# Kernel optimization log

Hardware: AMD Instinct MI355X
Metric: run time of the kernel (lower is better)

Reference implementation:

```python
import jax, jax.numpy as jnp
import numpy as np

D = 16       # data dimension
M = 64       # hidden width
ALPHA0 = 1.0 # alpha[0]
H_RES = 1.0  # ResNet step h = 1/(n_layers-1), n_layers=2


def _antideriv_tanh(x):
    # log(exp(x)+exp(-x)), numerically stable
    return jnp.abs(x) + jnp.log1p(jnp.exp(-2.0 * jnp.abs(x)))


def _dtanh(x):
    t = jnp.tanh(x)
    return 1.0 - t * t


def grad_and_hessian_trace(s, w, A, b, K0, b0, K1, b1):
    """OT-Flow analytic grad of Phi and trace of Hessian (w.r.t. first d coords).
    s: (n, d+1) = [x; t]. n_layers=2 -> one residual layer, h=1."""
    d = s.shape[1] - 1
    opening = s @ K0.T + b0                         # (n, m)
    u0 = _antideriv_tanh(opening)                   # (n, m)
    feat1 = u0 @ K1.T + b1                          # (n, m)
    tanhopen = jnp.tanh(opening)                    # (n, m)
    # backward pass for gradient: z1 = w + h K1^T (tanh(feat1) * w)
    z1 = w + H_RES * (jnp.tanh(feat1) * w) @ K1     # (n, m)
    z0 = (tanhopen * z1) @ K0                       # (n, d+1)
    symA = A.T @ A                                  # (d+1, d+1)
    grad = z0 + s @ symA + b                        # (n, d+1)
    # Hessian trace: opening-layer term
    Kopen = K0[:, :d]                               # (m, d)
    trH = (_dtanh(opening) * z1) @ jnp.sum(Kopen**2, axis=1)   # (n,)
    # forward-propagated Jacobian of u0 w.r.t. x: (n, m, d)
    Jac = tanhopen[:, :, None] * Kopen[None, :, :]
    KJ = jnp.einsum('ij,njd->nid', K1, Jac)         # (n, m, d)
    t1 = jnp.einsum('nm,nmd->n', _dtanh(feat1) * w, KJ**2)
    trH = trH + H_RES * t1 + jnp.sum(A[:, :d] ** 2)  # + trace(symA[:d,:d])
    return grad, trH


def odefun(z, t, w, A, b, K0, b0, K1, b1):
    n = z.shape[0]
    x = z[:, :D]
    s = jnp.concatenate([x, jnp.full((n, 1), t, dtype=z.dtype)], axis=1)
    gradPhi, trH = grad_and_hessian_trace(s, w, A, b, K0, b0, K1, b1)
    dx = -(1.0 / ALPHA0) * gradPhi[:, :D]
    dl = -(1.0 / ALPHA0) * trH[:, None]
    dv = 0.5 * jnp.sum(dx * dx, axis=1, keepdims=True)
    dr = jnp.abs(-gradPhi[:, -1:] + ALPHA0 * dv)
    return jnp.concatenate([dx, dl, dv, dr], axis=1)


def step_rk4(f, z, t0, t1):
    h = t1 - t0
    z0 = z
    K = h * f(z0, t0)
    z = z0 + K / 6.0
    K = h * f(z0 + 0.5 * K, t0 + 0.5 * h)
    z = z + K / 3.0
    K = h * f(z0 + 0.5 * K, t0 + 0.5 * h)
    z = z + K / 3.0
    K = h * f(z0 + K, t0 + h)
    z = z + K / 6.0
    return z


def setup_inputs() -> dict:
    key = jax.random.key(0)
    ks = jax.random.split(key, 8)
    n = 32768
    dp1 = D + 1
    x = jax.random.normal(ks[0], (n, D), dtype=jnp.float32)
    w = jax.random.normal(ks[1], (M,), dtype=jnp.float32) / np.sqrt(M)
    A = 0.1 * jax.random.normal(ks[2], (10, dp1), dtype=jnp.float32)
    b = 0.1 * jax.random.normal(ks[3], (dp1,), dtype=jnp.float32)
    K0 = jax.random.normal(ks[4], (M, dp1), dtype=jnp.float32) / np.sqrt(dp1)
    b0 = 0.1 * jax.random.normal(ks[5], (M,), dtype=jnp.float32)
    K1 = jax.random.normal(ks[6], (M, M), dtype=jnp.float32) / np.sqrt(M)
    b1 = 0.1 * jax.random.normal(ks[7], (M,), dtype=jnp.float32)
    return {"x": x, "w": w, "A": A, "b": b, "K0": K0, "b0": b0,
            "K1": K1, "b1": b1, "nt": 8}


def reference(x, w, A, b, K0, b0, K1, b1, nt):
    f = lambda z, t: odefun(z, t, w, A, b, K0, b0, K1, b1)
    h = 1.0 / nt
    z = jnp.concatenate([x, jnp.zeros((x.shape[0], 3), x.dtype)], axis=1)
    for k in range(nt):  # nt is a static python int
        z = step_rk4(f, z, k * h, (k + 1) * h)
    # unpack: (x_latent, log_det, transport_cost, hjb_violation)
    return z[:, :D], z[:, D], z[:, D + 1], z[:, D + 2]
```

## Files before the change

### kernel.cpp

```cpp
#include <hip/hip_runtime.h>
#include <math.h>

typedef __attribute__((ext_vector_type(8))) short bf16x8;
typedef __attribute__((ext_vector_type(4))) float f32x4;

union B8 { bf16x8 v; unsigned u[4]; };

__device__ __forceinline__ unsigned pk2(float lo, float hi) {
  unsigned r;
  asm("v_cvt_pk_bf16_f32 %0, %1, %2" : "=v"(r) : "v"(lo), "v"(hi));
  return r;
}
__device__ __forceinline__ float rcpf(float x) { return __builtin_amdgcn_rcpf(x); }
__device__ __forceinline__ void ldsfence() { asm volatile("s_waitcnt lgkmcnt(0)" ::: "memory"); }

#define MFMA __builtin_amdgcn_mfma_f32_16x16x32_bf16

__global__ void otflow_prep(const float* __restrict__ K0g,
                            const float* __restrict__ Ag,
                            float* __restrict__ ws) {
  __shared__ float Als[170];
  int tid = threadIdx.x;
  for (int idx = tid; idx < 1024; idx += 256) {
    int m = idx >> 4, d = idx & 15;
    ws[idx] = K0g[m * 17 + d];
  }
  if (tid < 170) Als[tid] = Ag[tid];
  if (tid < 64) {
    float s = 0.f;
    for (int d = 0; d < 16; ++d) { float v = K0g[tid * 17 + d]; s += v * v; }
    ws[1320 + tid] = s;
  }
  __syncthreads();
  for (int idx = tid; idx < 289; idx += 256) {
    int j = idx / 17, k2 = idx % 17;
    float s = 0.f;
#pragma unroll
    for (int r = 0; r < 10; ++r) s += Als[r * 17 + j] * Als[r * 17 + k2];
    ws[1024 + idx] = s;
  }
  __syncthreads();
  if (tid == 0) {
    float s = 0.f;
    for (int r = 0; r < 10; ++r)
      for (int j = 0; j < 16; ++j) { float v = Als[r * 17 + j]; s += v * v; }
    ws[1313] = s;
  }
}

__global__ __launch_bounds__(64, 2) void otflow_main(
    const float* __restrict__ xg, const float* __restrict__ wg,
    const float* __restrict__ bg, const float* __restrict__ K0g,
    const float* __restrict__ b0g, const float* __restrict__ K1g,
    const float* __restrict__ b1g, const int* __restrict__ ntg,
    const float* __restrict__ ws, float* __restrict__ out, int n) {
  __shared__ float buf[16 * 68];
  __shared__ float csh[16 * 68];
  __shared__ float qsh[16 * 68];
  __shared__ float tsh[16 * 20];
  __shared__ float b1s[64], wss[64], k0qs[64], b0s[64], tcs[64];

  const int lane = threadIdx.x;
  const int lr = lane & 15;
  const int lg = lane >> 4;

  b1s[lane] = b1g[lane];
  wss[lane] = wg[lane];
  k0qs[lane] = ws[1320 + lane];
  b0s[lane] = b0g[lane];
  tcs[lane] = K0g[lane * 17 + 16];

  const float sumA2 = ws[1313];

  B8 aK0[4], aK0L[4], aK1[8], aK1T[8], aG[6];
  float kop[16];
#pragma unroll
  for (int mi = 0; mi < 4; ++mi) {
    B8 th, tl;
#pragma unroll
    for (int jj = 0; jj < 4; ++jj) {
      float e0 = K0g[(mi * 16 + lr) * 17 + (lg & 1) * 8 + jj * 2];
      float e1 = K0g[(mi * 16 + lr) * 17 + (lg & 1) * 8 + jj * 2 + 1];
      unsigned hh = pk2(e0, e1);
      th.u[jj] = hh;
      float l0 = e0 - __uint_as_float(hh << 16);
      float l1 = e1 - __uint_as_float(hh & 0xffff0000u);
      tl.u[jj] = pk2(l0, l1);
    }
    aK0[mi] = th; aK0L[mi] = tl;
  }
#pragma unroll
  for (int mi = 0; mi < 4; ++mi)
#pragma unroll
    for (int kb = 0; kb < 2; ++kb) {
      const float* pp = K1g + (mi * 16 + lr) * 64 + kb * 32 + lg * 8;
      float4 q0 = *(const float4*)pp;
      float4 q1 = *(const float4*)(pp + 4);
      B8 t;
      t.u[0] = pk2(q0.x, q0.y); t.u[1] = pk2(q0.z, q0.w);
      t.u[2] = pk2(q1.x, q1.y); t.u[3] = pk2(q1.z, q1.w);
      aK1[mi * 2 + kb] = t;
    }
#pragma unroll
  for (int mi = 0; mi < 4; ++mi)
#pragma unroll
    for (int kb = 0; kb < 2; ++kb) {
      int ib = kb * 32 + lg * 8;
      int m = mi * 16 + lr;
      B8 t;
#pragma unroll
      for (int jj = 0; jj < 4; ++jj)
        t.u[jj] = pk2(K1g[(ib + jj * 2) * 64 + m], K1g[(ib + jj * 2 + 1) * 64 + m]);
      aK1T[mi * 2 + kb] = t;
    }
#pragma unroll
  for (int nb = 0; nb < 2; ++nb)
#pragma unroll
    for (int kb = 0; kb < 3; ++kb) {
      int j = nb * 16 + lr; if (j > 16) j = 16;
      float e[8];
#pragma unroll
      for (int jj = 0; jj < 8; ++jj) {
        float v;
        if (kb < 2) v = K0g[(kb * 32 + lg * 8 + jj) * 17 + j];
        else {
          int kr = lg * 8 + jj;
          v = (kr < 17) ? ws[1024 + kr * 17 + j] : (kr == 17) ? bg[j] : 0.f;
        }
        e[jj] = v;
      }
      B8 t;
      t.u[0] = pk2(e[0], e[1]); t.u[1] = pk2(e[2], e[3]);
      t.u[2] = pk2(e[4], e[5]); t.u[3] = pk2(e[6], e[7]);
      aG[nb * 3 + kb] = t;
    }
#pragma unroll
  for (int kb = 0; kb < 2; ++kb)
#pragma unroll
    for (int j = 0; j < 8; ++j)
      kop[kb * 8 + j] = ws[(kb * 32 + lg * 8 + j) * 16 + lr];

  ldsfence();

  const int nt = *ntg;
  const float h = 1.0f / (float)nt;
  const int p0 = blockIdx.x * 16;
  int pidx = p0 + lr; if (pidx >= n) pidx = n - 1;

  float xin[4], x0s[4], xac[4];
  {
    float4 xi = *(const float4*)(xg + (size_t)pidx * 16 + lg * 4);
    xin[0] = xi.x; xin[1] = xi.y; xin[2] = xi.z; xin[3] = xi.w;
#pragma unroll
    for (int r = 0; r < 4; ++r) { x0s[r] = xin[r]; xac[r] = xin[r]; }
  }
  float lacc = 0.f, vacc = 0.f, racc = 0.f;
  const f32x4 zz = {0.f, 0.f, 0.f, 0.f};

  for (int kstep = 0; kstep < nt; ++kstep) {
    float t0 = (float)kstep * h;
#pragma unroll 1
    for (int st = 0; st < 4; ++st) {
      float tin = t0 + ((st == 0) ? 0.f : (st == 3) ? h : 0.5f * h);

      { float4 xv = {xin[0], xin[1], xin[2], xin[3]};
        *(float4*)(buf + lr * 68 + lg * 4) = xv; }
      ldsfence();
      float4 s0 = *(const float4*)(buf + lr * 68 + (lg & 1) * 8);
      float4 s1 = *(const float4*)(buf + lr * 68 + (lg & 1) * 8 + 4);
      unsigned h0 = pk2(s0.x, s0.y), h1 = pk2(s0.z, s0.w);
      unsigned h2 = pk2(s1.x, s1.y), h3 = pk2(s1.z, s1.w);
      B8 sfO, sfG;
      if (lg < 2) {
        sfO.u[0] = h0; sfO.u[1] = h1; sfO.u[2] = h2; sfO.u[3] = h3;
        sfG.u[0] = h0; sfG.u[1] = h1; sfG.u[2] = h2; sfG.u[3] = h3;
      } else {
        float l0 = s0.x - __uint_as_float(h0 << 16);
        float l1 = s0.y - __uint_as_float(h0 & 0xffff0000u);
        float l2 = s0.z - __uint_as_float(h1 << 16);
        float l3 = s0.w - __uint_as_float(h1 & 0xffff0000u);
        float l4 = s1.x - __uint_as_float(h2 << 16);
        float l5 = s1.y - __uint_as_float(h2 & 0xffff0000u);
        float l6 = s1.z - __uint_as_float(h3 << 16);
        float l7 = s1.w - __uint_as_float(h3 & 0xffff0000u);
        sfO.u[0] = pk2(l0, l1); sfO.u[1] = pk2(l2, l3);
        sfO.u[2] = pk2(l4, l5); sfO.u[3] = pk2(l6, l7);
        if (lg == 2) { sfG.u[0] = pk2(tin, 1.f); sfG.u[1] = 0; sfG.u[2] = 0; sfG.u[3] = 0; }
        else { sfG.u[0] = 0; sfG.u[1] = 0; sfG.u[2] = 0; sfG.u[3] = 0; }
      }

      f32x4 o0 = MFMA(aK0[0].v, sfO.v, zz, 0, 0, 0);
      f32x4 o1 = MFMA(aK0[1].v, sfO.v, zz, 0, 0, 0);
      f32x4 o2 = MFMA(aK0[2].v, sfO.v, zz, 0, 0, 0);
      f32x4 o3 = MFMA(aK0[3].v, sfO.v, zz, 0, 0, 0);
      o0 = MFMA(aK0L[0].v, sfO.v, o0, 0, 0, 0);
      o1 = MFMA(aK0L[1].v, sfO.v, o1, 0, 0, 0);
      o2 = MFMA(aK0L[2].v, sfO.v, o2, 0, 0, 0);
      o3 = MFMA(aK0L[3].v, sfO.v, o3, 0, 0, 0);

      float cva[16];
#pragma unroll
      for (int mi = 0; mi < 4; ++mi) {
        f32x4 oa = (mi == 0) ? o0 : (mi == 1) ? o1 : (mi == 2) ? o2 : o3;
        float4 b0v = *(const float4*)(b0s + mi * 16 + lg * 4);
        float4 tcv = *(const float4*)(tcs + mi * 16 + lg * 4);
        float4 u0v;
#pragma unroll
        for (int r = 0; r < 4; ++r) {
          float ov = oa[r] + fmaf(tin, ((const float*)&tcv)[r], ((const float*)&b0v)[r]);
          float e = __expf(-2.f * fabsf(ov));
          float rp = rcpf(1.f + e);
          float cm = (1.f - e) * rp;
          cva[mi * 4 + r] = __builtin_copysignf(cm, ov);
          ((float*)&u0v)[r] = fabsf(ov) + __logf(1.f + e);
        }
        *(float4*)(buf + lr * 68 + mi * 16 + lg * 4) = u0v;
      }
      ldsfence();

      B8 uf0, uf1;
      {
        const float* bp = buf + lr * 68;
        float4 a0 = *(const float4*)(bp + lg * 8);
        float4 a1 = *(const float4*)(bp + lg * 8 + 4);
        float4 a2 = *(const float4*)(bp + 32 + lg * 8);
        float4 a3 = *(const float4*)(bp + 32 + lg * 8 + 4);
        uf0.u[0] = pk2(a0.x, a0.y); uf0.u[1] = pk2(a0.z, a0.w);
        uf0.u[2] = pk2(a1.x, a1.y); uf0.u[3] = pk2(a1.z, a1.w);
        uf1.u[0] = pk2(a2.x, a2.y); uf1.u[1] = pk2(a2.z, a2.w);
        uf1.u[2] = pk2(a3.x, a3.y); uf1.u[3] = pk2(a3.z, a3.w);
      }
      f32x4 f0 = MFMA(aK1[0].v, uf0.v, zz, 0, 0, 0); f0 = MFMA(aK1[1].v, uf1.v, f0, 0, 0, 0);
      f32x4 f1 = MFMA(aK1[2].v, uf0.v, zz, 0, 0, 0); f1 = MFMA(aK1[3].v, uf1.v, f1, 0, 0, 0);
      f32x4 f2 = MFMA(aK1[4].v, uf0.v, zz, 0, 0, 0); f2 = MFMA(aK1[5].v, uf1.v, f2, 0, 0, 0);
      f32x4 f3 = MFMA(aK1[6].v, uf0.v, zz, 0, 0, 0); f3 = MFMA(aK1[7].v, uf1.v, f3, 0, 0, 0);

#pragma unroll
      for (int mi = 0; mi < 4; ++mi) {
        f32x4 fa = (mi == 0) ? f0 : (mi == 1) ? f1 : (mi == 2) ? f2 : f3;
        float4 b1v = *(const float4*)(b1s + mi * 16 + lg * 4);
        float4 wv = *(const float4*)(wss + mi * 16 + lg * 4);
        float4 av4, qv4;
#pragma unroll
        for (int r = 0; r < 4; ++r) {
          float fv = fa[r] + ((const float*)&b1v)[r];
          float e = __expf(-2.f * fabsf(fv));
          float rp = rcpf(1.f + e);
          float tf = __builtin_copysignf((1.f - e) * rp, fv);
          float wr = ((const float*)&wv)[r];
          ((float*)&av4)[r] = tf * wr;
          ((float*)&qv4)[r] = (1.f - tf * tf) * wr;
        }
        *(float4*)(buf + lr * 68 + mi * 16 + lg * 4) = av4;
        *(float4*)(qsh + lr * 68 + mi * 16 + lg * 4) = qv4;
      }
      ldsfence();

      B8 af0, af1;
      {
        const float* bp = buf + lr * 68;
        float4 a0 = *(const float4*)(bp + lg * 8);
        float4 a1 = *(const float4*)(bp + lg * 8 + 4);
        float4 a2 = *(const float4*)(bp + 32 + lg * 8);
        float4 a3 = *(const float4*)(bp + 32 + lg * 8 + 4);
        af0.u[0] = pk2(a0.x, a0.y); af0.u[1] = pk2(a0.z, a0.w);
        af0.u[2] = pk2(a1.x, a1.y); af0.u[3] = pk2(a1.z, a1.w);
        af1.u[0] = pk2(a2.x, a2.y); af1.u[1] = pk2(a2.z, a2.w);
        af1.u[2] = pk2(a3.x, a3.y); af1.u[3] = pk2(a3.z, a3.w);
      }
      f32x4 z0 = MFMA(aK1T[0].v, af0.v, zz, 0, 0, 0); z0 = MFMA(aK1T[1].v, af1.v, z0, 0, 0, 0);
      f32x4 z1 = MFMA(aK1T[2].v, af0.v, zz, 0, 0, 0); z1 = MFMA(aK1T[3].v, af1.v, z1, 0, 0, 0);
      f32x4 z2 = MFMA(aK1T[4].v, af0.v, zz, 0, 0, 0); z2 = MFMA(aK1T[5].v, af1.v, z2, 0, 0, 0);
      f32x4 z3 = MFMA(aK1T[6].v, af0.v, zz, 0, 0, 0); z3 = MFMA(aK1T[7].v, af1.v, z3, 0, 0, 0);

      float trh_l = 0.f;
#pragma unroll
      for (int mi = 0; mi < 4; ++mi) {
        f32x4 za = (mi == 0) ? z0 : (mi == 1) ? z1 : (mi == 2) ? z2 : z3;
        float4 wv = *(const float4*)(wss + mi * 16 + lg * 4);
        float4 kq = *(const float4*)(k0qs + mi * 16 + lg * 4);
        float4 rv4, cv4;
#pragma unroll
        for (int r = 0; r < 4; ++r) {
          float c = cva[mi * 4 + r];
          float z1v = za[r] + ((const float*)&wv)[r];
          ((float*)&rv4)[r] = c * z1v;
          float dt0 = 1.f - c * c;
          trh_l = fmaf(dt0 * z1v, ((const float*)&kq)[r], trh_l);
          ((float*)&cv4)[r] = c;
        }
        *(float4*)(buf + lr * 68 + mi * 16 + lg * 4) = rv4;
        *(float4*)(csh + lr * 68 + mi * 16 + lg * 4) = cv4;
      }
      trh_l += __shfl_xor(trh_l, 16, 64);
      trh_l += __shfl_xor(trh_l, 32, 64);
      ldsfence();

#pragma unroll 2
      for (int p = 0; p < 16; ++p) {
        const float* cp = csh + p * 68;
        float4 ca = *(const float4*)(cp + lg * 8);
        float4 cb = *(const float4*)(cp + lg * 8 + 4);
        float4 cc = *(const float4*)(cp + 32 + lg * 8);
        float4 cd = *(const float4*)(cp + 32 + lg * 8 + 4);
        B8 y0, y1;
        y0.u[0] = pk2(ca.x * kop[0], ca.y * kop[1]);
        y0.u[1] = pk2(ca.z * kop[2], ca.w * kop[3]);
        y0.u[2] = pk2(cb.x * kop[4], cb.y * kop[5]);
        y0.u[3] = pk2(cb.z * kop[6], cb.w * kop[7]);
        y1.u[0] = pk2(cc.x * kop[8], cc.y * kop[9]);
        y1.u[1] = pk2(cc.z * kop[10], cc.w * kop[11]);
        y1.u[2] = pk2(cd.x * kop[12], cd.y * kop[13]);
        y1.u[3] = pk2(cd.z * kop[14], cd.w * kop[15]);
        f32x4 kc0 = MFMA(y0.v, aK1[0].v, zz, 0, 0, 0); kc0 = MFMA(y1.v, aK1[1].v, kc0, 0, 0, 0);
        f32x4 kc1 = MFMA(y0.v, aK1[2].v, zz, 0, 0, 0); kc1 = MFMA(y1.v, aK1[3].v, kc1, 0, 0, 0);
        f32x4 kc2 = MFMA(y0.v, aK1[4].v, zz, 0, 0, 0); kc2 = MFMA(y1.v, aK1[5].v, kc2, 0, 0, 0);
        f32x4 kc3 = MFMA(y0.v, aK1[6].v, zz, 0, 0, 0); kc3 = MFMA(y1.v, aK1[7].v, kc3, 0, 0, 0);
        float q0 = qsh[p * 68 + lr];
        float q1 = qsh[p * 68 + 16 + lr];
        float q2 = qsh[p * 68 + 32 + lr];
        float q3 = qsh[p * 68 + 48 + lr];
        float d0 = kc0[0] * kc0[0] + kc0[1] * kc0[1] + kc0[2] * kc0[2] + kc0[3] * kc0[3];
        float d1 = kc1[0] * kc1[0] + kc1[1] * kc1[1] + kc1[2] * kc1[2] + kc1[3] * kc1[3];
        float d2 = kc2[0] * kc2[0] + kc2[1] * kc2[1] + kc2[2] * kc2[2] + kc2[3] * kc2[3];
        float d3 = kc3[0] * kc3[0] + kc3[1] * kc3[1] + kc3[2] * kc3[2] + kc3[3] * kc3[3];
        float tp = q0 * d0 + q1 * d1 + q2 * d2 + q3 * d3;
        tp += __shfl_xor(tp, 16, 64);
        tp += __shfl_xor(tp, 32, 64);
        if (lg == 0) tsh[p * 20 + lr] = tp;
      }
      ldsfence();
      float4 tv = *(const float4*)(tsh + lr * 20 + lg * 4);
      float tsum = tv.x + tv.y + tv.z + tv.w;
      tsum += __shfl_xor(tsum, 16, 64);
      tsum += __shfl_xor(tsum, 32, 64);

      B8 rf0, rf1;
      {
        const float* bp = buf + lr * 68;
        float4 a0 = *(const float4*)(bp + lg * 8);
        float4 a1 = *(const float4*)(bp + lg * 8 + 4);
        float4 a2 = *(const float4*)(bp + 32 + lg * 8);
        float4 a3 = *(const float4*)(bp + 32 + lg * 8 + 4);
        rf0.u[0] = pk2(a0.x, a0.y); rf0.u[1] = pk2(a0.z, a0.w);
        rf0.u[2] = pk2(a1.x, a1.y); rf0.u[3] = pk2(a1.z, a1.w);
        rf1.u[0] = pk2(a2.x, a2.y); rf1.u[1] = pk2(a2.z, a2.w);
        rf1.u[2] = pk2(a3.x, a3.y); rf1.u[3] = pk2(a3.z, a3.w);
      }
      f32x4 g0 = MFMA(aG[0].v, rf0.v, zz, 0, 0, 0);
      g0 = MFMA(aG[1].v, rf1.v, g0, 0, 0, 0);
      g0 = MFMA(aG[2].v, sfG.v, g0, 0, 0, 0);
      f32x4 g1 = MFMA(aG[3].v, rf0.v, zz, 0, 0, 0);
      g1 = MFMA(aG[4].v, rf1.v, g1, 0, 0, 0);
      g1 = MFMA(aG[5].v, sfG.v, g1, 0, 0, 0);

      float kx[4];
      float dvp = 0.f;
#pragma unroll
      for (int r = 0; r < 4; ++r) { float d = -g0[r]; kx[r] = d; dvp = fmaf(d, d, dvp); }
      dvp += __shfl_xor(dvp, 16, 64);
      dvp += __shfl_xor(dvp, 32, 64);
      dvp *= 0.5f;
      float g16 = g1[0];
      float trH = trh_l + tsum + sumA2;
      float dl = -trH;
      float dr = fabsf(dvp - g16);
      float wch = ((st == 0 || st == 3) ? (1.f / 6.f) : (1.f / 3.f)) * h;
#pragma unroll
      for (int r = 0; r < 4; ++r) xac[r] = fmaf(wch, kx[r], xac[r]);
      lacc = fmaf(wch, dl, lacc);
      vacc = fmaf(wch, dvp, vacc);
      racc = fmaf(wch, dr, racc);
      if (st < 3) {
        float anh = ((st == 2) ? 1.f : 0.5f) * h;
#pragma unroll
        for (int r = 0; r < 4; ++r) xin[r] = fmaf(anh, kx[r], x0s[r]);
      } else {
#pragma unroll
        for (int r = 0; r < 4; ++r) { x0s[r] = xac[r]; xin[r] = xac[r]; }
      }
    }
  }

  if (p0 + lr < n) {
    float4 xa = {xac[0], xac[1], xac[2], xac[3]};
    *(float4*)(out + (size_t)(p0 + lr) * 16 + lg * 4) = xa;
    if (lg == 0) {
      out[(size_t)n * 16 + p0 + lr] = lacc;
      out[(size_t)n * 17 + p0 + lr] = vacc;
      out[(size_t)n * 18 + p0 + lr] = racc;
    }
  }
}

extern "C" void kernel_launch(void* const* d_in, const int* in_sizes, int n_in,
                              void* d_out, int out_size, void* d_ws, size_t ws_size,
                              hipStream_t stream) {
  const float* xg = (const float*)d_in[0];
  const float* wg = (const float*)d_in[1];
  const float* Ag = (const float*)d_in[2];
  const float* bg = (const float*)d_in[3];
  const float* K0g = (const float*)d_in[4];
  const float* b0g = (const float*)d_in[5];
  const float* K1g = (const float*)d_in[6];
  const float* b1g = (const float*)d_in[7];
  const int* ntg = (const int*)d_in[8];
  float* out = (float*)d_out;
  float* ws = (float*)d_ws;
  int n = in_sizes[0] / 16;

  hipLaunchKernelGGL(otflow_prep, dim3(1), dim3(256), 0, stream, K0g, Ag, ws);
  int nblk = (n + 15) / 16;
  hipLaunchKernelGGL(otflow_main, dim3(nblk), dim3(64), 0, stream,
                     xg, wg, bg, K0g, b0g, K1g, b1g, ntg, ws, out, n);
}
```

Measured before the change: 358.3 us.

## Split each block into two waves of eight samples with shared K0 fragments in LDS

Result: slower. 689.7 us (+92.5%).

```diff
diff --git a/kernel.cpp b/kernel.cpp
--- a/kernel.cpp
+++ b/kernel.cpp
@@ -3,12 +3,19 @@
 
 typedef __attribute__((ext_vector_type(8))) short bf16x8;
 typedef __attribute__((ext_vector_type(4))) float f32x4;
-
-union B8 { bf16x8 v; unsigned u[4]; };
+typedef __attribute__((ext_vector_type(2))) float f32x2;
+typedef __attribute__((ext_vector_type(4))) unsigned u32x4;
+
+union B8 { bf16x8 v; unsigned u[4]; u32x4 q; };
 
 __device__ __forceinline__ unsigned pk2(float lo, float hi) {
   unsigned r;
   asm("v_cvt_pk_bf16_f32 %0, %1, %2" : "=v"(r) : "v"(lo), "v"(hi));
+  return r;
+}
+__device__ __forceinline__ f32x2 pkmul(f32x2 a, f32x2 b) {
+  f32x2 r;
+  asm("v_pk_mul_f32 %0, %1, %2" : "=v"(r) : "v"(a), "v"(b));
   return r;
 }
 __device__ __forceinline__ float rcpf(float x) { return __builtin_amdgcn_rcpf(x); }
@@ -48,47 +55,57 @@
   }
 }
 
-__global__ __launch_bounds__(64, 2) void otflow_main(
+__global__ __launch_bounds__(128, 3) void otflow_main(
     const float* __restrict__ xg, const float* __restrict__ wg,
     const float* __restrict__ bg, const float* __restrict__ K0g,
     const float* __restrict__ b0g, const float* __restrict__ K1g,
     const float* __restrict__ b1g, const int* __restrict__ ntg,
     const float* __restrict__ ws, float* __restrict__ out, int n) {
-  __shared__ float buf[16 * 68];
-  __shared__ float csh[16 * 68];
-  __shared__ float qsh[16 * 68];
-  __shared__ float tsh[16 * 20];
-  __shared__ float b1s[64], wss[64], k0qs[64], b0s[64], tcs[64];
-
-  const int lane = threadIdx.x;
+  __shared__ unsigned aK0lds[8 * 64 * 4];
+  __shared__ unsigned Xu[2][8 * 36];
+  __shared__ float csh[2][8 * 68];
+  __shared__ float qsh[2][8 * 68];
+  __shared__ float gsh[2][8 * 20];
+  __shared__ float tshv[2][8];
+  __shared__ float b0s[64], tcs[64], b1s[64], wss[64], k0qs[64], scol[18];
+
+  const int tid = threadIdx.x;
+  const int wid = tid >> 6;
+  const int lane = tid & 63;
   const int lr = lane & 15;
   const int lg = lane >> 4;
-
-  b1s[lane] = b1g[lane];
-  wss[lane] = wg[lane];
-  k0qs[lane] = ws[1320 + lane];
-  b0s[lane] = b0g[lane];
-  tcs[lane] = K0g[lane * 17 + 16];
+  const int p8 = lr & 7;
+  const bool own = (lr < 8);
+
+  if (wid == 0) {
+    b0s[lane] = b0g[lane];
+    tcs[lane] = K0g[lane * 17 + 16];
+    b1s[lane] = b1g[lane];
+    wss[lane] = wg[lane];
+    k0qs[lane] = ws[1320 + lane];
+    if (lane < 17) scol[lane] = ws[1024 + lane * 17 + 16];
+    if (lane == 17) scol[17] = bg[16];
+#pragma unroll
+    for (int mi = 0; mi < 4; ++mi) {
+      unsigned th[4], tl[4];
+#pragma unroll
+      for (int jj = 0; jj < 4; ++jj) {
+        float e0 = K0g[(mi * 16 + lr) * 17 + (lg & 1) * 8 + jj * 2];
+        float e1 = K0g[(mi * 16 + lr) * 17 + (lg & 1) * 8 + jj * 2 + 1];
+        unsigned hh = pk2(e0, e1);
+        th[jj] = hh;
+        float l0 = e0 - __uint_as_float(hh << 16);
+        float l1 = e1 - __uint_as_float(hh & 0xffff0000u);
+        tl[jj] = pk2(l0, l1);
+      }
+      *(u32x4*)(aK0lds + (mi * 64 + lane) * 4) = (u32x4){th[0], th[1], th[2], th[3]};
+      *(u32x4*)(aK0lds + ((4 + mi) * 64 + lane) * 4) = (u32x4){tl[0], tl[1], tl[2], tl[3]};
+    }
+  }
 
   const float sumA2 = ws[1313];
 
-  B8 aK0[4], aK0L[4], aK1[8], aK1T[8], aG[6];
-  float kop[16];
-#pragma unroll
-  for (int mi = 0; mi < 4; ++mi) {
-    B8 th, tl;
-#pragma unroll
-    for (int jj = 0; jj < 4; ++jj) {
-      float e0 = K0g[(mi * 16 + lr) * 17 + (lg & 1) * 8 + jj * 2];
-      float e1 = K0g[(mi * 16 + lr) * 17 + (lg & 1) * 8 + jj * 2 + 1];
-      unsigned hh = pk2(e0, e1);
-      th.u[jj] = hh;
-      float l0 = e0 - __uint_as_float(hh << 16);
-      float l1 = e1 - __uint_as_float(hh & 0xffff0000u);
-      tl.u[jj] = pk2(l0, l1);
-    }
-    aK0[mi] = th; aK0L[mi] = tl;
-  }
+  B8 aK1[8];
 #pragma unroll
   for (int mi = 0; mi < 4; ++mi)
 #pragma unroll
@@ -101,23 +118,24 @@
       t.u[2] = pk2(q1.x, q1.y); t.u[3] = pk2(q1.z, q1.w);
       aK1[mi * 2 + kb] = t;
     }
+  B8 aK1T[8];
 #pragma unroll
   for (int mi = 0; mi < 4; ++mi)
 #pragma unroll
     for (int kb = 0; kb < 2; ++kb) {
       int ib = kb * 32 + lg * 8;
       int m = mi * 16 + lr;
-      B8 t;
+      B8 tt;
 #pragma unroll
       for (int jj = 0; jj < 4; ++jj)
-        t.u[jj] = pk2(K1g[(ib + jj * 2) * 64 + m], K1g[(ib + jj * 2 + 1) * 64 + m]);
-      aK1T[mi * 2 + kb] = t;
-    }
-#pragma unroll
-  for (int nb = 0; nb < 2; ++nb)
+        tt.u[jj] = pk2(K1g[(ib + jj * 2) * 64 + m], K1g[(ib + jj * 2 + 1) * 64 + m]);
+      aK1T[mi * 2 + kb] = tt;
+    }
+  B8 aG0[3];
+  {
+    int j = lr;
 #pragma unroll
     for (int kb = 0; kb < 3; ++kb) {
-      int j = nb * 16 + lr; if (j > 16) j = 16;
       float e[8];
 #pragma unroll
       for (int jj = 0; jj < 8; ++jj) {
@@ -132,20 +150,29 @@
       B8 t;
       t.u[0] = pk2(e[0], e[1]); t.u[1] = pk2(e[2], e[3]);
       t.u[2] = pk2(e[4], e[5]); t.u[3] = pk2(e[6], e[7]);
-      aG[nb * 3 + kb] = t;
-    }
+      aG0[kb] = t;
+    }
+  }
+  f32x2 kop2[8];
 #pragma unroll
   for (int kb = 0; kb < 2; ++kb)
 #pragma unroll
-    for (int j = 0; j < 8; ++j)
-      kop[kb * 8 + j] = ws[(kb * 32 + lg * 8 + j) * 16 + lr];
-
-  ldsfence();
+    for (int j = 0; j < 4; ++j) {
+      f32x2 t;
+      t.x = ws[(kb * 32 + lg * 8 + 2 * j) * 16 + lr];
+      t.y = ws[(kb * 32 + lg * 8 + 2 * j + 1) * 16 + lr];
+      kop2[kb * 4 + j] = t;
+    }
+
+  __syncthreads();
+
+  float4 sc4 = *(const float4*)(scol + lg * 4);
+  const float sc16 = scol[16], sc17 = scol[17];
 
   const int nt = *ntg;
   const float h = 1.0f / (float)nt;
-  const int p0 = blockIdx.x * 16;
-  int pidx = p0 + lr; if (pidx >= n) pidx = n - 1;
+  const int pbase = blockIdx.x * 16 + wid * 8;
+  int pidx = pbase + p8; if (pidx >= n) pidx = n - 1;
 
   float xin[4], x0s[4], xac[4];
   {
@@ -156,6 +183,11 @@
   }
   float lacc = 0.f, vacc = 0.f, racc = 0.f;
   const f32x4 zz = {0.f, 0.f, 0.f, 0.f};
+
+  unsigned* Xw = Xu[wid];
+  float* cw = csh[wid];
+  float* qw = qsh[wid];
+  float* gw = gsh[wid];
 
   for (int kstep = 0; kstep < nt; ++kstep) {
     float t0 = (float)kstep * h;
@@ -163,11 +195,14 @@
     for (int st = 0; st < 4; ++st) {
       float tin = t0 + ((st == 0) ? 0.f : (st == 3) ? h : 0.5f * h);
 
-      { float4 xv = {xin[0], xin[1], xin[2], xin[3]};
-        *(float4*)(buf + lr * 68 + lg * 4) = xv; }
+      if (own) {
+        float4 xv = {xin[0], xin[1], xin[2], xin[3]};
+        *(float4*)(cw + p8 * 68 + lg * 4) = xv;
+      }
       ldsfence();
-      float4 s0 = *(const float4*)(buf + lr * 68 + (lg & 1) * 8);
-      float4 s1 = *(const float4*)(buf + lr * 68 + (lg & 1) * 8 + 4);
+      const float* sp = cw + p8 * 68;
+      float4 s0 = *(const float4*)(sp + (lg & 1) * 8);
+      float4 s1 = *(const float4*)(sp + (lg & 1) * 8 + 4);
       unsigned h0 = pk2(s0.x, s0.y), h1 = pk2(s0.z, s0.w);
       unsigned h2 = pk2(s1.x, s1.y), h3 = pk2(s1.z, s1.w);
       B8 sfO, sfG;
@@ -189,179 +224,168 @@
         else { sfG.u[0] = 0; sfG.u[1] = 0; sfG.u[2] = 0; sfG.u[3] = 0; }
       }
 
-      f32x4 o0 = MFMA(aK0[0].v, sfO.v, zz, 0, 0, 0);
-      f32x4 o1 = MFMA(aK0[1].v, sfO.v, zz, 0, 0, 0);
-      f32x4 o2 = MFMA(aK0[2].v, sfO.v, zz, 0, 0, 0);
-      f32x4 o3 = MFMA(aK0[3].v, sfO.v, zz, 0, 0, 0);
-      o0 = MFMA(aK0L[0].v, sfO.v, o0, 0, 0, 0);
-      o1 = MFMA(aK0L[1].v, sfO.v, o1, 0, 0, 0);
-      o2 = MFMA(aK0L[2].v, sfO.v, o2, 0, 0, 0);
-      o3 = MFMA(aK0L[3].v, sfO.v, o3, 0, 0, 0);
-
-      float cva[16];
-#pragma unroll
-      for (int mi = 0; mi < 4; ++mi) {
-        f32x4 oa = (mi == 0) ? o0 : (mi == 1) ? o1 : (mi == 2) ? o2 : o3;
+      B8 k0f[8];
+#pragma unroll
+      for (int f = 0; f < 8; ++f) k0f[f].q = *(const u32x4*)(aK0lds + (f * 64 + lane) * 4);
+      f32x4 oA[4];
+#pragma unroll
+      for (int mi = 0; mi < 4; ++mi) {
+        oA[mi] = MFMA(k0f[mi].v, sfO.v, zz, 0, 0, 0);
+        oA[mi] = MFMA(k0f[4 + mi].v, sfO.v, oA[mi], 0, 0, 0);
+      }
+#pragma unroll
+      for (int mi = 0; mi < 4; ++mi) {
         float4 b0v = *(const float4*)(b0s + mi * 16 + lg * 4);
         float4 tcv = *(const float4*)(tcs + mi * 16 + lg * 4);
-        float4 u0v;
+        float u0v[4], cv[4];
 #pragma unroll
         for (int r = 0; r < 4; ++r) {
-          float ov = oa[r] + fmaf(tin, ((const float*)&tcv)[r], ((const float*)&b0v)[r]);
+          float ov = oA[mi][r] + fmaf(tin, ((const float*)&tcv)[r], ((const float*)&b0v)[r]);
           float e = __expf(-2.f * fabsf(ov));
           float rp = rcpf(1.f + e);
-          float cm = (1.f - e) * rp;
-          cva[mi * 4 + r] = __builtin_copysignf(cm, ov);
-          ((float*)&u0v)[r] = fabsf(ov) + __logf(1.f + e);
-        }
-        *(float4*)(buf + lr * 68 + mi * 16 + lg * 4) = u0v;
+          cv[r] = __builtin_copysignf((1.f - e) * rp, ov);
+          u0v[r] = fabsf(ov) + __logf(1.f + e);
+        }
+        unsigned ua = pk2(u0v[0], u0v[1]), ub = pk2(u0v[2], u0v[3]);
+        if (own) {
+          *(uint2*)(Xw + p8 * 36 + mi * 8 + lg * 2) = make_uint2(ua, ub);
+          float4 cf = {cv[0], cv[1], cv[2], cv[3]};
+          *(float4*)(cw + p8 * 68 + mi * 16 + lg * 4) = cf;
+        }
       }
       ldsfence();
 
       B8 uf0, uf1;
-      {
-        const float* bp = buf + lr * 68;
-        float4 a0 = *(const float4*)(bp + lg * 8);
-        float4 a1 = *(const float4*)(bp + lg * 8 + 4);
-        float4 a2 = *(const float4*)(bp + 32 + lg * 8);
-        float4 a3 = *(const float4*)(bp + 32 + lg * 8 + 4);
-        uf0.u[0] = pk2(a0.x, a0.y); uf0.u[1] = pk2(a0.z, a0.w);
-        uf0.u[2] = pk2(a1.x, a1.y); uf0.u[3] = pk2(a1.z, a1.w);
-        uf1.u[0] = pk2(a2.x, a2.y); uf1.u[1] = pk2(a2.z, a2.w);
-        uf1.u[2] = pk2(a3.x, a3.y); uf1.u[3] = pk2(a3.z, a3.w);
-      }
-      f32x4 f0 = MFMA(aK1[0].v, uf0.v, zz, 0, 0, 0); f0 = MFMA(aK1[1].v, uf1.v, f0, 0, 0, 0);
-      f32x4 f1 = MFMA(aK1[2].v, uf0.v, zz, 0, 0, 0); f1 = MFMA(aK1[3].v, uf1.v, f1, 0, 0, 0);
-      f32x4 f2 = MFMA(aK1[4].v, uf0.v, zz, 0, 0, 0); f2 = MFMA(aK1[5].v, uf1.v, f2, 0, 0, 0);
-      f32x4 f3 = MFMA(aK1[6].v, uf0.v, zz, 0, 0, 0); f3 = MFMA(aK1[7].v, uf1.v, f3, 0, 0, 0);
-
-#pragma unroll
-      for (int mi = 0; mi < 4; ++mi) {
-        f32x4 fa = (mi == 0) ? f0 : (mi == 1) ? f1 : (mi == 2) ? f2 : f3;
+      uf0.q = *(const u32x4*)(Xw + p8 * 36 + lg * 4);
+      uf1.q = *(const u32x4*)(Xw + p8 * 36 + 16 + lg * 4);
+      f32x4 fA[4];
+#pragma unroll
+      for (int mi = 0; mi < 4; ++mi) {
+        fA[mi] = MFMA(aK1[mi * 2].v, uf0.v, zz, 0, 0, 0);
+        fA[mi] = MFMA(aK1[mi * 2 + 1].v, uf1.v, fA[mi], 0, 0, 0);
+      }
+#pragma unroll
+      for (int mi = 0; mi < 4; ++mi) {
         float4 b1v = *(const float4*)(b1s + mi * 16 + lg * 4);
         float4 wv = *(const float4*)(wss + mi * 16 + lg * 4);
-        float4 av4, qv4;
+        float av[4], qv[4];
 #pragma unroll
         for (int r = 0; r < 4; ++r) {
-          float fv = fa[r] + ((const float*)&b1v)[r];
+          float fv = fA[mi][r] + ((const float*)&b1v)[r];
           float e = __expf(-2.f * fabsf(fv));
           float rp = rcpf(1.f + e);
           float tf = __builtin_copysignf((1.f - e) * rp, fv);
           float wr = ((const float*)&wv)[r];
-          ((float*)&av4)[r] = tf * wr;
-          ((float*)&qv4)[r] = (1.f - tf * tf) * wr;
-        }
-        *(float4*)(buf + lr * 68 + mi * 16 + lg * 4) = av4;
-        *(float4*)(qsh + lr * 68 + mi * 16 + lg * 4) = qv4;
+          av[r] = tf * wr;
+          qv[r] = (1.f - tf * tf) * wr;
+        }
+        unsigned pa = pk2(av[0], av[1]), pb = pk2(av[2], av[3]);
+        if (own) {
+          *(uint2*)(Xw + p8 * 36 + mi * 8 + lg * 2) = make_uint2(pa, pb);
+          float4 qf = {qv[0], qv[1], qv[2], qv[3]};
+          *(float4*)(qw + p8 * 68 + mi * 16 + lg * 4) = qf;
+        }
       }
       ldsfence();
 
       B8 af0, af1;
-      {
-        const float* bp = buf + lr * 68;
-        float4 a0 = *(const float4*)(bp + lg * 8);
-        float4 a1 = *(const float4*)(bp + lg * 8 + 4);
-        float4 a2 = *(const float4*)(bp + 32 + lg * 8);
-        float4 a3 = *(const float4*)(bp + 32 + lg * 8 + 4);
-        af0.u[0] = pk2(a0.x, a0.y); af0.u[1] = pk2(a0.z, a0.w);
-        af0.u[2] = pk2(a1.x, a1.y); af0.u[3] = pk2(a1.z, a1.w);
-        af1.u[0] = pk2(a2.x, a2.y); af1.u[1] = pk2(a2.z, a2.w);
-        af1.u[2] = pk2(a3.x, a3.y); af1.u[3] = pk2(a3.z, a3.w);
-      }
-      f32x4 z0 = MFMA(aK1T[0].v, af0.v, zz, 0, 0, 0); z0 = MFMA(aK1T[1].v, af1.v, z0, 0, 0, 0);
-      f32x4 z1 = MFMA(aK1T[2].v, af0.v, zz, 0, 0, 0); z1 = MFMA(aK1T[3].v, af1.v, z1, 0, 0, 0);
-      f32x4 z2 = MFMA(aK1T[4].v, af0.v, zz, 0, 0, 0); z2 = MFMA(aK1T[5].v, af1.v, z2, 0, 0, 0);
-      f32x4 z3 = MFMA(aK1T[6].v, af0.v, zz, 0, 0, 0); z3 = MFMA(aK1T[7].v, af1.v, z3, 0, 0, 0);
-
-      float trh_l = 0.f;
-#pragma unroll
-      for (int mi = 0; mi < 4; ++mi) {
-        f32x4 za = (mi == 0) ? z0 : (mi == 1) ? z1 : (mi == 2) ? z2 : z3;
+      af0.q = *(const u32x4*)(Xw + p8 * 36 + lg * 4);
+      af1.q = *(const u32x4*)(Xw + p8 * 36 + 16 + lg * 4);
+      f32x4 zA[4];
+#pragma unroll
+      for (int mi = 0; mi < 4; ++mi) {
+        zA[mi] = MFMA(aK1T[mi * 2].v, af0.v, zz, 0, 0, 0);
+        zA[mi] = MFMA(aK1T[mi * 2 + 1].v, af1.v, zA[mi], 0, 0, 0);
+      }
+      float trh_l = 0.f, g16p = 0.f;
+#pragma unroll
+      for (int mi = 0; mi < 4; ++mi) {
         float4 wv = *(const float4*)(wss + mi * 16 + lg * 4);
         float4 kq = *(const float4*)(k0qs + mi * 16 + lg * 4);
-        float4 rv4, cv4;
+        float4 tcv = *(const float4*)(tcs + mi * 16 + lg * 4);
+        float4 cv4 = *(const float4*)(cw + p8 * 68 + mi * 16 + lg * 4);
+        float rv[4];
 #pragma unroll
         for (int r = 0; r < 4; ++r) {
-          float c = cva[mi * 4 + r];
-          float z1v = za[r] + ((const float*)&wv)[r];
-          ((float*)&rv4)[r] = c * z1v;
-          float dt0 = 1.f - c * c;
-          trh_l = fmaf(dt0 * z1v, ((const float*)&kq)[r], trh_l);
-          ((float*)&cv4)[r] = c;
-        }
-        *(float4*)(buf + lr * 68 + mi * 16 + lg * 4) = rv4;
-        *(float4*)(csh + lr * 68 + mi * 16 + lg * 4) = cv4;
-      }
+          float c = ((const float*)&cv4)[r];
+          float z1v = zA[mi][r] + ((const float*)&wv)[r];
+          rv[r] = c * z1v;
+          trh_l = fmaf((1.f - c * c) * z1v, ((const float*)&kq)[r], trh_l);
+          g16p = fmaf(rv[r], ((const float*)&tcv)[r], g16p);
+        }
+        unsigned ra = pk2(rv[0], rv[1]), rb = pk2(rv[2], rv[3]);
+        if (own) *(uint2*)(Xw + p8 * 36 + mi * 8 + lg * 2) = make_uint2(ra, rb);
+      }
+#pragma unroll
+      for (int r = 0; r < 4; ++r) g16p = fmaf(xin[r], ((const float*)&sc4)[r], g16p);
       trh_l += __shfl_xor(trh_l, 16, 64);
       trh_l += __shfl_xor(trh_l, 32, 64);
+      g16p += __shfl_xor(g16p, 16, 64);
+      g16p += __shfl_xor(g16p, 32, 64);
+      float g16 = g16p + fmaf(tin, sc16, sc17);
       ldsfence();
 
 #pragma unroll 2
-      for (int p = 0; p < 16; ++p) {
-        const float* cp = csh + p * 68;
+      for (int p = 0; p < 8; ++p) {
+        const float* cp = cw + p * 68;
         float4 ca = *(const float4*)(cp + lg * 8);
         float4 cb = *(const float4*)(cp + lg * 8 + 4);
         float4 cc = *(const float4*)(cp + 32 + lg * 8);
         float4 cd = *(const float4*)(cp + 32 + lg * 8 + 4);
         B8 y0, y1;
-        y0.u[0] = pk2(ca.x * kop[0], ca.y * kop[1]);
-        y0.u[1] = pk2(ca.z * kop[2], ca.w * kop[3]);
-        y0.u[2] = pk2(cb.x * kop[4], cb.y * kop[5]);
-        y0.u[3] = pk2(cb.z * kop[6], cb.w * kop[7]);
-        y1.u[0] = pk2(cc.x * kop[8], cc.y * kop[9]);
-        y1.u[1] = pk2(cc.z * kop[10], cc.w * kop[11]);
-        y1.u[2] = pk2(cd.x * kop[12], cd.y * kop[13]);
-        y1.u[3] = pk2(cd.z * kop[14], cd.w * kop[15]);
+        f32x2 pr;
+        pr = pkmul((f32x2){ca.x, ca.y}, kop2[0]); y0.u[0] = pk2(pr.x, pr.y);
+        pr = pkmul((f32x2){ca.z, ca.w}, kop2[1]); y0.u[1] = pk2(pr.x, pr.y);
+        pr = pkmul((f32x2){cb.x, cb.y}, kop2[2]); y0.u[2] = pk2(pr.x, pr.y);
+        pr = pkmul((f32x2){cb.z, cb.w}, kop2[3]); y0.u[3] = pk2(pr.x, pr.y);
+        pr = pkmul((f32x2){cc.x, cc.y}, kop2[4]); y1.u[0] = pk2(pr.x, pr.y);
+        pr = pkmul((f32x2){cc.z, cc.w}, kop2[5]); y1.u[1] = pk2(pr.x, pr.y);
+        pr = pkmul((f32x2){cd.x, cd.y}, kop2[6]); y1.u[2] = pk2(pr.x, pr.y);
+        pr = pkmul((f32x2){cd.z, cd.w}, kop2[7]); y1.u[3] = pk2(pr.x, pr.y);
         f32x4 kc0 = MFMA(y0.v, aK1[0].v, zz, 0, 0, 0); kc0 = MFMA(y1.v, aK1[1].v, kc0, 0, 0, 0);
         f32x4 kc1 = MFMA(y0.v, aK1[2].v, zz, 0, 0, 0); kc1 = MFMA(y1.v, aK1[3].v, kc1, 0, 0, 0);
         f32x4 kc2 = MFMA(y0.v, aK1[4].v, zz, 0, 0, 0); kc2 = MFMA(y1.v, aK1[5].v, kc2, 0, 0, 0);
         f32x4 kc3 = MFMA(y0.v, aK1[6].v, zz, 0, 0, 0); kc3 = MFMA(y1.v, aK1[7].v, kc3, 0, 0, 0);
-        float q0 = qsh[p * 68 + lr];
-        float q1 = qsh[p * 68 + 16 + lr];
-        float q2 = qsh[p * 68 + 32 + lr];
-        float q3 = qsh[p * 68 + 48 + lr];
+        float q0 = qw[p * 68 + lr];
+        float q1 = qw[p * 68 + 16 + lr];
+        float q2 = qw[p * 68 + 32 + lr];
+        float q3 = qw[p * 68 + 48 + lr];
         float d0 = kc0[0] * kc0[0] + kc0[1] * kc0[1] + kc0[2] * kc0[2] + kc0[3] * kc0[3];
         float d1 = kc1[0] * kc1[0] + kc1[1] * kc1[1] + kc1[2] * kc1[2] + kc1[3] * kc1[3];
         float d2 = kc2[0] * kc2[0] + kc2[1] * kc2[1] + kc2[2] * kc2[2] + kc2[3] * kc2[3];
         float d3 = kc3[0] * kc3[0] + kc3[1] * kc3[1] + kc3[2] * kc3[2] + kc3[3] * kc3[3];
         float tp = q0 * d0 + q1 * d1 + q2 * d2 + q3 * d3;
-        tp += __shfl_xor(tp, 16, 64);
-        tp += __shfl_xor(tp, 32, 64);
-        if (lg == 0) tsh[p * 20 + lr] = tp;
+#pragma unroll
+        for (int off = 1; off < 64; off <<= 1) tp += __shfl_xor(tp, off, 64);
+        if (lane == 0) tshv[wid][p] = tp;
+      }
+
+      {
+        B8 rf0, rf1;
+        rf0.q = *(const u32x4*)(Xw + p8 * 36 + lg * 4);
+        rf1.q = *(const u32x4*)(Xw + p8 * 36 + 16 + lg * 4);
+        f32x4 g = MFMA(aG0[0].v, rf0.v, zz, 0, 0, 0);
+        g = MFMA(aG0[1].v, rf1.v, g, 0, 0, 0);
+        g = MFMA(aG0[2].v, sfG.v, g, 0, 0, 0);
+        if (own) {
+          float4 gf = {g[0], g[1], g[2], g[3]};
+          *(float4*)(gw + p8 * 20 + lg * 4) = gf;
+        }
       }
       ldsfence();
-      float4 tv = *(const float4*)(tsh + lr * 20 + lg * 4);
-      float tsum = tv.x + tv.y + tv.z + tv.w;
-      tsum += __shfl_xor(tsum, 16, 64);
-      tsum += __shfl_xor(tsum, 32, 64);
-
-      B8 rf0, rf1;
-      {
-        const float* bp = buf + lr * 68;
-        float4 a0 = *(const float4*)(bp + lg * 8);
-        float4 a1 = *(const float4*)(bp + lg * 8 + 4);
-        float4 a2 = *(const float4*)(bp + 32 + lg * 8);
-        float4 a3 = *(const float4*)(bp + 32 + lg * 8 + 4);
-        rf0.u[0] = pk2(a0.x, a0.y); rf0.u[1] = pk2(a0.z, a0.w);
-        rf0.u[2] = pk2(a1.x, a1.y); rf0.u[3] = pk2(a1.z, a1.w);
-        rf1.u[0] = pk2(a2.x, a2.y); rf1.u[1] = pk2(a2.z, a2.w);
-        rf1.u[2] = pk2(a3.x, a3.y); rf1.u[3] = pk2(a3.z, a3.w);
-      }
-      f32x4 g0 = MFMA(aG[0].v, rf0.v, zz, 0, 0, 0);
-      g0 = MFMA(aG[1].v, rf1.v, g0, 0, 0, 0);
-      g0 = MFMA(aG[2].v, sfG.v, g0, 0, 0, 0);
-      f32x4 g1 = MFMA(aG[3].v, rf0.v, zz, 0, 0, 0);
-      g1 = MFMA(aG[4].v, rf1.v, g1, 0, 0, 0);
-      g1 = MFMA(aG[5].v, sfG.v, g1, 0, 0, 0);
-
+
+      float tsum = tshv[wid][p8];
+      float4 gv = *(const float4*)(gw + p8 * 20 + lg * 4);
       float kx[4];
       float dvp = 0.f;
 #pragma unroll
-      for (int r = 0; r < 4; ++r) { float d = -g0[r]; kx[r] = d; dvp = fmaf(d, d, dvp); }
+      for (int r = 0; r < 4; ++r) {
+        float d = -((const float*)&gv)[r];
+        kx[r] = d; dvp = fmaf(d, d, dvp);
+      }
       dvp += __shfl_xor(dvp, 16, 64);
       dvp += __shfl_xor(dvp, 32, 64);
       dvp *= 0.5f;
-      float g16 = g1[0];
       float trH = trh_l + tsum + sumA2;
       float dl = -trH;
       float dr = fabsf(dvp - g16);
@@ -382,13 +406,14 @@
     }
   }
 
-  if (p0 + lr < n) {
+  int pi = pbase + p8;
+  if (own && pi < n) {
     float4 xa = {xac[0], xac[1], xac[2], xac[3]};
-    *(float4*)(out + (size_t)(p0 + lr) * 16 + lg * 4) = xa;
+    *(float4*)(out + (size_t)pi * 16 + lg * 4) = xa;
     if (lg == 0) {
-      out[(size_t)n * 16 + p0 + lr] = lacc;
-      out[(size_t)n * 17 + p0 + lr] = vacc;
-      out[(size_t)n * 18 + p0 + lr] = racc;
+      out[(size_t)n * 16 + pi] = lacc;
+      out[(size_t)n * 17 + pi] = vacc;
+      out[(size_t)n * 18 + pi] = racc;
     }
   }
 }
@@ -411,6 +436,6 @@
 
   hipLaunchKernelGGL(otflow_prep, dim3(1), dim3(256), 0, stream, K0g, Ag, ws);
   int nblk = (n + 15) / 16;
-  hipLaunchKernelGGL(otflow_main, dim3(nblk), dim3(64), 0, stream,
+  hipLaunchKernelGGL(otflow_main, dim3(nblk), dim3(128), 0, stream,
                      xg, wg, bg, K0g, b0g, K1g, b1g, ntg, ws, out, n);
 }
```
